# Performance work log

Hardware: AMD Instinct MI355X
Metric: run time of the kernel (lower is better)

## Reference

```python
import jax, jax.numpy as jnp
import numpy as np

N_NODES = 100000
FEAT_DIM = 256
EMBED_DIM = 256
BATCH = 50000
NUM_SAMPLE = 25
NAN_FILL = 0.01  # neigh_feats[isnan] = 0.01 in the original


def setup_inputs() -> dict:
    key = jax.random.key(0)
    k1, k2, k3, k4 = jax.random.split(key, 4)
    features = jax.random.normal(k1, (N_NODES, FEAT_DIM), dtype=jnp.float32)
    # Xavier-uniform-ish weight [embed_dim, feat_dim + embed_dim] (gcn=True)
    fan = FEAT_DIM + EMBED_DIM
    bound = float(np.sqrt(6.0 / (EMBED_DIM + fan)))
    weight = jax.random.uniform(k2, (EMBED_DIM, fan), dtype=jnp.float32,
                                minval=-bound, maxval=bound)
    nodes = jax.random.randint(k3, (BATCH,), 0, N_NODES, dtype=jnp.int64)
    neigh_idx = jax.random.randint(k4, (BATCH, NUM_SAMPLE), 0, N_NODES, dtype=jnp.int64)
    return {"features": features, "weight": weight, "nodes": nodes,
            "neigh_idx": neigh_idx}


def reference(features, weight, nodes, neigh_idx):
    # MeanAggregator: gather sampled neighbor features and mean over neighbors
    neigh_feats = features[neigh_idx].mean(axis=1)            # [B, F]
    neigh_feats = jnp.where(jnp.isnan(neigh_feats), NAN_FILL, neigh_feats)
    self_feats = features[nodes]                              # [B, F]
    combined = jnp.concatenate([self_feats, neigh_feats], axis=1)  # [B, F+E]
    # weight.matmul(combined.t()) then ReLU -> [E, B]
    out = jax.nn.relu(jnp.einsum('ef,bf->eb', weight, combined))
    return out
```

## Files before the change

kernel.cpp:

```cpp
#include <hip/hip_runtime.h>
#include <hip/hip_bf16.h>
#include <hip/hip_fp8.h>

#define FEAT    256
#define KDIM    512
#define EMBED   256
#define BATCH   50000
#define NSAMP   25
#define N_NODES 100000
#define NAN_FILL 0.01f

#define NTILE   48
#define LSTRIDE 520

typedef __attribute__((ext_vector_type(8))) short  short8;
typedef __attribute__((ext_vector_type(4))) float  floatx4;
typedef __attribute__((ext_vector_type(4))) unsigned short ushort4v;
typedef __attribute__((ext_vector_type(4))) float  float4v;

__device__ inline unsigned short f2bf(float x) {
    __hip_bfloat16 h = __float2bfloat16(x);
    union { __hip_bfloat16 h; unsigned short u; } c; c.h = h;
    return c.u;
}
__device__ inline unsigned char f2fp8(float x) {
    __hip_fp8_e4m3 t(x);
    return (unsigned char)t.__x;
}
__device__ inline float fp8f(unsigned v) {
    __hip_fp8_e4m3 t; t.__x = (unsigned char)v;
    return (float)t;
}

__global__ __launch_bounds__(256) void fconv8_kernel(
    const float* __restrict__ F, unsigned char* __restrict__ F8)
{
    const size_t i = ((size_t)blockIdx.x * 256 + threadIdx.x) * 8;
    float4v a = *(const float4v*)(F + i);
    float4v b = *(const float4v*)(F + i + 4);
    union { unsigned char c[8]; uint2 v; } o;
    o.c[0] = f2fp8(a[0]); o.c[1] = f2fp8(a[1]); o.c[2] = f2fp8(a[2]); o.c[3] = f2fp8(a[3]);
    o.c[4] = f2fp8(b[0]); o.c[5] = f2fp8(b[1]); o.c[6] = f2fp8(b[2]); o.c[7] = f2fp8(b[3]);
    *(uint2*)(F8 + i) = o.v;
}

__global__ __launch_bounds__(256) void wconv_kernel(
    const float* __restrict__ W, unsigned short* __restrict__ Wb)
{
    const int i = blockIdx.x * 256 + threadIdx.x;
    Wb[i] = f2bf(W[i]);
}

__global__ __launch_bounds__(256, 3) void enc_kernel(
    const float* __restrict__ F,
    const unsigned char* __restrict__ F8,
    const unsigned short* __restrict__ Wb,
    const int* __restrict__ nodes,
    const int* __restrict__ neigh,
    float* __restrict__ out)
{
    __shared__ unsigned short cl[NTILE * LSTRIDE];

    const int lane = threadIdx.x & 63;
    const int wave = threadIdx.x >> 6;
    const int q = lane >> 4;
    const int r = lane & 15;
    const int nbase = blockIdx.x * NTILE;

    for (int it = 0; it < NTILE / 4; ++it) {
        const int li = wave * (NTILE / 4) + it;
        int b = nbase + li;
        if (b >= BATCH) b = BATCH - 1;

        const int node = nodes[b];
        float4v sv = *(const float4v*)(F + (size_t)node * FEAT + lane * 4);

        const int* nb = neigh + (size_t)b * NSAMP;
        float s0 = 0.f, s1 = 0.f, s2 = 0.f, s3 = 0.f;
        #pragma unroll
        for (int j = 0; j < NSAMP; ++j) {
            const int idx = nb[j];
            unsigned wv = *(const unsigned*)(F8 + (size_t)idx * FEAT + lane * 4);
            s0 += fp8f(wv);
            s1 += fp8f(wv >> 8);
            s2 += fp8f(wv >> 16);
            s3 += fp8f(wv >> 24);
        }
        const float inv = 1.0f / NSAMP;
        float m0 = s0 * inv, m1 = s1 * inv, m2 = s2 * inv, m3 = s3 * inv;
        if (m0 != m0) m0 = NAN_FILL;
        if (m1 != m1) m1 = NAN_FILL;
        if (m2 != m2) m2 = NAN_FILL;
        if (m3 != m3) m3 = NAN_FILL;

        unsigned short* row = cl + li * LSTRIDE;
        ushort4v s; s[0] = f2bf(sv[0]); s[1] = f2bf(sv[1]); s[2] = f2bf(sv[2]); s[3] = f2bf(sv[3]);
        *(ushort4v*)(row + lane * 4) = s;
        ushort4v m; m[0] = f2bf(m0); m[1] = f2bf(m1); m[2] = f2bf(m2); m[3] = f2bf(m3);
        *(ushort4v*)(row + FEAT + lane * 4) = m;
    }
    __syncthreads();

    const int mbase = wave * 64;
    const short* Wp = (const short*)Wb;
    const short* cp = (const short*)cl;

    floatx4 acc[4][3] = {};

    for (int k = 0; k < KDIM; k += 32) {
        short8 afr[4], bfr[3];
        #pragma unroll
        for (int mt = 0; mt < 4; ++mt) {
            const short* p = Wp + (size_t)(mbase + mt * 16 + r) * KDIM + k + q * 8;
            afr[mt] = *(const short8*)p;
        }
        #pragma unroll
        for (int nt = 0; nt < 3; ++nt) {
            const short* p = cp + (nt * 16 + r) * LSTRIDE + k + q * 8;
            bfr[nt] = *(const short8*)p;
        }
        #pragma unroll
        for (int mt = 0; mt < 4; ++mt)
            #pragma unroll
            for (int nt = 0; nt < 3; ++nt)
                acc[mt][nt] = __builtin_amdgcn_mfma_f32_16x16x32_bf16(
                    afr[mt], bfr[nt], acc[mt][nt], 0, 0, 0);
    }

    #pragma unroll
    for (int mt = 0; mt < 4; ++mt) {
        #pragma unroll
        for (int nt = 0; nt < 3; ++nt) {
            const int col = nbase + nt * 16 + r;
            if (col < BATCH) {
                #pragma unroll
                for (int i = 0; i < 4; ++i) {
                    const int row = mbase + mt * 16 + q * 4 + i;
                    float v = acc[mt][nt][i];
                    out[(size_t)row * BATCH + col] = v > 0.f ? v : 0.f;
                }
            }
        }
    }
}

extern "C" void kernel_launch(void* const* d_in, const int* in_sizes, int n_in,
                              void* d_out, int out_size, void* d_ws, size_t ws_size,
                              hipStream_t stream) {
    const float* features = (const float*)d_in[0];
    const float* weight   = (const float*)d_in[1];
    const int*   nodes    = (const int*)d_in[2];
    const int*   neigh    = (const int*)d_in[3];
    float* out = (float*)d_out;

    unsigned char* F8  = (unsigned char*)d_ws;
    unsigned short* Wb = (unsigned short*)(F8 + (size_t)N_NODES * FEAT);

    fconv8_kernel<<<(N_NODES * FEAT) / (256 * 8), 256, 0, stream>>>(features, F8);
    wconv_kernel<<<(EMBED * KDIM) / 256, 256, 0, stream>>>(weight, Wb);

    const int nblocks = (BATCH + NTILE - 1) / NTILE;
    enc_kernel<<<nblocks, 256, 0, stream>>>(features, F8, Wb, nodes, neigh, out);
}
```

Measured before the change: 257.9 us.

## Use 8 waves per block and packed FP8 conversion builtins

Doubles the block to 512 threads (8 waves), so each wave gathers 6 rows instead of 12 and computes a 32-row slice of the output instead of 64. This gives more waves in flight to hide the latency of the random gathers. It also swaps the scalar FP8 encode and decode for packed cvt_pk builtins when they are available, which cuts ALU work in the conversion kernel and the gather loop. The cost is that each wave now loads fewer A fragments per B fragment it loads, so weight reuse per wave drops, and the occupancy request of 6 blocks of 512 threads may constrain registers.

```diff
diff --git a/kernel.cpp b/kernel.cpp
--- a/kernel.cpp
+++ b/kernel.cpp
@@ -11,12 +11,25 @@
 #define NAN_FILL 0.01f
 
 #define NTILE   48
+#define NWAVES  8
 #define LSTRIDE 520
 
 typedef __attribute__((ext_vector_type(8))) short  short8;
 typedef __attribute__((ext_vector_type(4))) float  floatx4;
+typedef __attribute__((ext_vector_type(2))) float  float2v;
 typedef __attribute__((ext_vector_type(4))) unsigned short ushort4v;
 typedef __attribute__((ext_vector_type(4))) float  float4v;
+
+#if __has_builtin(__builtin_amdgcn_cvt_pk_f32_fp8)
+#define PK_FP8_DEC 1
+#else
+#define PK_FP8_DEC 0
+#endif
+#if __has_builtin(__builtin_amdgcn_cvt_pk_fp8_f32)
+#define PK_FP8_ENC 1
+#else
+#define PK_FP8_ENC 0
+#endif
 
 __device__ inline unsigned short f2bf(float x) {
     __hip_bfloat16 h = __float2bfloat16(x);
@@ -38,10 +51,19 @@
     const size_t i = ((size_t)blockIdx.x * 256 + threadIdx.x) * 8;
     float4v a = *(const float4v*)(F + i);
     float4v b = *(const float4v*)(F + i + 4);
+#if PK_FP8_ENC
+    unsigned w0 = (unsigned)__builtin_amdgcn_cvt_pk_fp8_f32(a[0], a[1], 0, false);
+    w0 = (unsigned)__builtin_amdgcn_cvt_pk_fp8_f32(a[2], a[3], (int)w0, true);
+    unsigned w1 = (unsigned)__builtin_amdgcn_cvt_pk_fp8_f32(b[0], b[1], 0, false);
+    w1 = (unsigned)__builtin_amdgcn_cvt_pk_fp8_f32(b[2], b[3], (int)w1, true);
+    uint2 o; o.x = w0; o.y = w1;
+    *(uint2*)(F8 + i) = o;
+#else
     union { unsigned char c[8]; uint2 v; } o;
     o.c[0] = f2fp8(a[0]); o.c[1] = f2fp8(a[1]); o.c[2] = f2fp8(a[2]); o.c[3] = f2fp8(a[3]);
     o.c[4] = f2fp8(b[0]); o.c[5] = f2fp8(b[1]); o.c[6] = f2fp8(b[2]); o.c[7] = f2fp8(b[3]);
     *(uint2*)(F8 + i) = o.v;
+#endif
 }
 
 __global__ __launch_bounds__(256) void wconv_kernel(
@@ -51,7 +73,7 @@
     Wb[i] = f2bf(W[i]);
 }
 
-__global__ __launch_bounds__(256, 3) void enc_kernel(
+__global__ __launch_bounds__(512, 6) void enc_kernel(
     const float* __restrict__ F,
     const unsigned char* __restrict__ F8,
     const unsigned short* __restrict__ Wb,
@@ -67,8 +89,8 @@
     const int r = lane & 15;
     const int nbase = blockIdx.x * NTILE;
 
-    for (int it = 0; it < NTILE / 4; ++it) {
-        const int li = wave * (NTILE / 4) + it;
+    for (int it = 0; it < NTILE / NWAVES; ++it) {
+        const int li = wave * (NTILE / NWAVES) + it;
         int b = nbase + li;
         if (b >= BATCH) b = BATCH - 1;
 
@@ -76,18 +98,23 @@
         float4v sv = *(const float4v*)(F + (size_t)node * FEAT + lane * 4);
 
         const int* nb = neigh + (size_t)b * NSAMP;
-        float s0 = 0.f, s1 = 0.f, s2 = 0.f, s3 = 0.f;
+        float2v s01 = {0.f, 0.f}, s23 = {0.f, 0.f};
         #pragma unroll
         for (int j = 0; j < NSAMP; ++j) {
             const int idx = nb[j];
             unsigned wv = *(const unsigned*)(F8 + (size_t)idx * FEAT + lane * 4);
-            s0 += fp8f(wv);
-            s1 += fp8f(wv >> 8);
-            s2 += fp8f(wv >> 16);
-            s3 += fp8f(wv >> 24);
+#if PK_FP8_DEC
+            s01 += __builtin_amdgcn_cvt_pk_f32_fp8((int)wv, false);
+            s23 += __builtin_amdgcn_cvt_pk_f32_fp8((int)wv, true);
+#else
+            s01[0] += fp8f(wv);
+            s01[1] += fp8f(wv >> 8);
+            s23[0] += fp8f(wv >> 16);
+            s23[1] += fp8f(wv >> 24);
+#endif
         }
         const float inv = 1.0f / NSAMP;
-        float m0 = s0 * inv, m1 = s1 * inv, m2 = s2 * inv, m3 = s3 * inv;
+        float m0 = s01[0] * inv, m1 = s01[1] * inv, m2 = s23[0] * inv, m3 = s23[1] * inv;
         if (m0 != m0) m0 = NAN_FILL;
         if (m1 != m1) m1 = NAN_FILL;
         if (m2 != m2) m2 = NAN_FILL;
@@ -101,16 +128,16 @@
     }
     __syncthreads();
 
-    const int mbase = wave * 64;
+    const int mbase = wave * 32;
     const short* Wp = (const short*)Wb;
     const short* cp = (const short*)cl;
 
-    floatx4 acc[4][3] = {};
+    floatx4 acc[2][3] = {};
 
     for (int k = 0; k < KDIM; k += 32) {
-        short8 afr[4], bfr[3];
+        short8 afr[2], bfr[3];
         #pragma unroll
-        for (int mt = 0; mt < 4; ++mt) {
+        for (int mt = 0; mt < 2; ++mt) {
             const short* p = Wp + (size_t)(mbase + mt * 16 + r) * KDIM + k + q * 8;
             afr[mt] = *(const short8*)p;
         }
@@ -120,7 +147,7 @@
             bfr[nt] = *(const short8*)p;
         }
         #pragma unroll
-        for (int mt = 0; mt < 4; ++mt)
+        for (int mt = 0; mt < 2; ++mt)
             #pragma unroll
             for (int nt = 0; nt < 3; ++nt)
                 acc[mt][nt] = __builtin_amdgcn_mfma_f32_16x16x32_bf16(
@@ -128,7 +155,7 @@
     }
 
     #pragma unroll
-    for (int mt = 0; mt < 4; ++mt) {
+    for (int mt = 0; mt < 2; ++mt) {
         #pragma unroll
         for (int nt = 0; nt < 3; ++nt) {
             const int col = nbase + nt * 16 + r;
@@ -160,5 +187,5 @@
     wconv_kernel<<<(EMBED * KDIM) / 256, 256, 0, stream>>>(weight, Wb);
 
     const int nblocks = (BATCH + NTILE - 1) / NTILE;
-    enc_kernel<<<nblocks, 256, 0, stream>>>(features, F8, Wb, nodes, neigh, out);
+    enc_kernel<<<nblocks, 512, 0, stream>>>(features, F8, Wb, nodes, neigh, out);
 }
```

Result: slower. 310.4 us (+20.4%).
